# Kernel optimization log

Hardware: AMD Instinct MI355X
Metric: run time of the kernel (lower is better)

The kernel has to match this reference:

```python
import jax, jax.numpy as jnp
import numpy as np

N = 100000
E = 1600000
IN_C, HID_C, OUT_C = 512, 128, 40
K = 5
ALPHA = 0.5


def setup_inputs() -> dict:
    key = jax.random.key(0)
    k1, k2, k3, k4, k5, k6 = jax.random.split(key, 6)
    x = jax.random.normal(k1, (N, IN_C), dtype=jnp.float32)
    edge_index = jax.random.randint(k2, (2, E), 0, N, dtype=jnp.int64)
    # lin1: in -> hidden, lin2: hidden -> out (Kaiming-uniform-ish scale)
    W1 = jax.random.normal(k3, (IN_C, HID_C), dtype=jnp.float32) * (1.0 / np.sqrt(IN_C))
    b1 = jax.random.normal(k4, (HID_C,), dtype=jnp.float32) * 0.01
    W2 = jax.random.normal(k5, (HID_C, OUT_C), dtype=jnp.float32) * (1.0 / np.sqrt(HID_C))
    b2 = jax.random.normal(k6, (OUT_C,), dtype=jnp.float32) * 0.01
    return {"x": x, "edge_index": edge_index, "W1": W1, "b1": b1, "W2": W2, "b2": b2}


def _gcn_norm(edge_index, num_nodes):
    # add self-loops with weight 1, then symmetric normalization D^-1/2 A D^-1/2
    loops = jnp.arange(num_nodes, dtype=edge_index.dtype)
    row = jnp.concatenate([edge_index[0], loops])
    col = jnp.concatenate([edge_index[1], loops])
    w = jnp.ones(row.shape[0], dtype=jnp.float32)
    deg = jax.ops.segment_sum(w, col, num_segments=num_nodes)
    dinv = jnp.where(deg > 0, jax.lax.rsqrt(deg), 0.0)
    norm = dinv[row] * w * dinv[col]
    return row, col, norm


def reference(x, edge_index, W1, b1, W2, b2):
    h = x @ W1 + b1                      # [N, HID_C]
    row, col, norm = _gcn_norm(edge_index, N)
    x0 = h
    for _ in range(K):
        # gather source features, scale by edge norm, scatter-add to targets
        agg = jax.ops.segment_sum(norm[:, None] * h[row], col, num_segments=N)
        h = (1.0 - ALPHA) * agg + ALPHA * x0
    return h @ W2 + b2                   # [N, OUT_C]
```

## Files before the change

### kernel.cpp

```cpp
#include <hip/hip_runtime.h>
#include <hip/hip_bf16.h>

#define NN 100000
#define EE 1600000
#define HALFN 50000

typedef __attribute__((ext_vector_type(8))) short short8;
typedef __attribute__((ext_vector_type(4))) float f32x4;

__device__ __forceinline__ short f2bf(float f) {
    __hip_bfloat16 h = __float2bfloat16(f);
    return *reinterpret_cast<short*>(&h);
}
__device__ __forceinline__ float bf2f(unsigned short u) {
    return __uint_as_float((unsigned int)u << 16);
}


__global__ void wct_kernel(const float* __restrict__ W1, const float* __restrict__ W2,
                           const float* __restrict__ b1, short* __restrict__ WcT,
                           float* __restrict__ bc) {
    int t = blockIdx.x * 256 + threadIdx.x;
    if (t < 48 * 512) {
        int j = t >> 9, k = t & 511;
        float s = 0.f;
        if (j < 40)
            for (int i = 0; i < 128; ++i) s = fmaf(W1[k * 128 + i], W2[i * 40 + j], s);
        WcT[j * 512 + k] = f2bf(s);
    } else if (t < 48 * 512 + 48) {
        int j = t - 48 * 512;
        float s = 0.f;
        if (j < 40)
            for (int i = 0; i < 128; ++i) s = fmaf(b1[i], W2[i * 40 + j], s);
        bc[j] = s;
    }
}

__global__ __launch_bounds__(256) void gemm_z0(const float* __restrict__ x,
                                               const short* __restrict__ WcT,
                                               const float* __restrict__ bc,
                                               unsigned short* __restrict__ z0) {
    const int tid = threadIdx.x;
    const int lane = tid & 63;
    const int wave = tid >> 6;
    const int rbase = blockIdx.x * 64 + wave * 16;
    const int row = rbase + (lane & 15);
    const int kc = lane >> 4;
    const bool rok = row < NN;

    f32x4 acc0 = {0.f, 0.f, 0.f, 0.f};
    f32x4 acc1 = {0.f, 0.f, 0.f, 0.f};
    f32x4 acc2 = {0.f, 0.f, 0.f, 0.f};

    const float* xrow = x + (size_t)row * 512 + kc * 8;
    const short* bp0 = WcT + (size_t)(lane & 15) * 512 + kc * 8;
    const short* bp1 = bp0 + 16 * 512;
    const short* bp2 = bp0 + 32 * 512;

    for (int k0 = 0; k0 < 512; k0 += 32) {
        float4 p0 = {0.f, 0.f, 0.f, 0.f}, p1 = {0.f, 0.f, 0.f, 0.f};
        if (rok) {
            p0 = *reinterpret_cast<const float4*>(xrow + k0);
            p1 = *reinterpret_cast<const float4*>(xrow + k0 + 4);
        }
        short8 a;
        a[0] = f2bf(p0.x); a[1] = f2bf(p0.y); a[2] = f2bf(p0.z); a[3] = f2bf(p0.w);
        a[4] = f2bf(p1.x); a[5] = f2bf(p1.y); a[6] = f2bf(p1.z); a[7] = f2bf(p1.w);
        short8 b0 = *reinterpret_cast<const short8*>(bp0 + k0);
        short8 b1 = *reinterpret_cast<const short8*>(bp1 + k0);
        short8 b2 = *reinterpret_cast<const short8*>(bp2 + k0);
        acc0 = __builtin_amdgcn_mfma_f32_16x16x32_bf16(a, b0, acc0, 0, 0, 0);
        acc1 = __builtin_amdgcn_mfma_f32_16x16x32_bf16(a, b1, acc1, 0, 0, 0);
        acc2 = __builtin_amdgcn_mfma_f32_16x16x32_bf16(a, b2, acc2, 0, 0, 0);
    }

    const int cb = lane & 15;
    const int rr = rbase + (lane >> 4) * 4;
#pragma unroll
    for (int q = 0; q < 4; ++q) {
        int r = rr + q;
        if (r < NN) {
            z0[(size_t)r * 64 + cb] = (unsigned short)f2bf(acc0[q] + bc[cb]);
            z0[(size_t)r * 64 + cb + 16] = (unsigned short)f2bf(acc1[q] + bc[cb + 16]);
            z0[(size_t)r * 64 + cb + 32] = (unsigned short)f2bf(acc2[q] + bc[cb + 32]);
        }
    }
}

__global__ void count_kernel(const int* __restrict__ eidx, int* __restrict__ counts) {
    int e = blockIdx.x * 256 + threadIdx.x;
    if (e < EE) atomicAdd(&counts[eidx[EE + e]], 1);
}

__global__ void scan1(const int* __restrict__ counts, int* __restrict__ ptr,
                      int* __restrict__ bsum) {
    __shared__ int s[256];
    int tid = threadIdx.x;
    int i = blockIdx.x * 256 + tid;
    int v = (i < NN) ? counts[i] : 0;
    s[tid] = v;
    __syncthreads();
    for (int off = 1; off < 256; off <<= 1) {
        int t = (tid >= off) ? s[tid - off] : 0;
        __syncthreads();
        s[tid] += t;
        __syncthreads();
    }
    if (i < NN) ptr[i] = s[tid] - v;
    if (tid == 255) bsum[blockIdx.x] = s[255];
}

__global__ void scan2(int* __restrict__ bsum) {
    __shared__ int s[512];
    int tid = threadIdx.x;
    int v = (tid < 391) ? bsum[tid] : 0;
    s[tid] = v;
    __syncthreads();
    for (int off = 1; off < 512; off <<= 1) {
        int t = (tid >= off) ? s[tid - off] : 0;
        __syncthreads();
        s[tid] += t;
        __syncthreads();
    }
    if (tid < 391) bsum[tid] = s[tid] - v;
}

__global__ void scan3(int* __restrict__ ptr, const int* __restrict__ bsum,
                      const int* __restrict__ counts, float* __restrict__ dinvp) {
    int i = blockIdx.x * 256 + threadIdx.x;
    if (i < NN) {
        ptr[i] += bsum[blockIdx.x];
        dinvp[i] = rsqrtf(1.0f + (float)counts[i]);
    }
    if (i == 0) ptr[NN] = EE;
}

__global__ void scatter_kernel(const int* __restrict__ eidx, const int* __restrict__ ptr,
                               const float* __restrict__ dinvp, int* __restrict__ cursor,
                               int2* __restrict__ cev) {
    int e = blockIdx.x * 256 + threadIdx.x;
    if (e < EE) {
        int r = eidx[e];
        int c = eidx[EE + e];
        int pos = ptr[c] + atomicAdd(&cursor[c], 1);
        cev[pos] = make_int2(r, __float_as_int(dinvp[r]));
    }
}

__global__ __launch_bounds__(256) void propagate(const unsigned short* __restrict__ zcur,
                                                 const unsigned short* __restrict__ z0q,
                                                 unsigned short* __restrict__ znb,
                                                 float* __restrict__ outf,
                                                 const int* __restrict__ ptr,
                                                 const int2* __restrict__ cev,
                                                 const float* __restrict__ dinvp,
                                                 const float* __restrict__ b2, int last) {
    const int lane = threadIdx.x & 63;
    const int wid = blockIdx.x * 4 + (threadIdx.x >> 6);
    const int n0 = wid, n1 = wid + HALFN;

    const int beg0 = ptr[n0], end0 = ptr[n0 + 1];
    const int beg1 = ptr[n1], end1 = ptr[n1 + 1];
    const float dc0 = dinvp[n0], dc1 = dinvp[n1];

    int m0 = end0 - beg0; if (m0 > 64) m0 = 64;
    int m1 = end1 - beg1; if (m1 > 64) m1 = 64;
    int2 ev0 = make_int2(0, 0), ev1 = make_int2(0, 0);
    if (m0 > 0) ev0 = cev[beg0 + (lane < m0 ? lane : m0 - 1)];
    if (m1 > 0) ev1 = cev[beg1 + (lane < m1 ? lane : m1 - 1)];
    const float self0 = bf2f(zcur[(size_t)n0 * 64 + lane]);
    const float self1 = bf2f(zcur[(size_t)n1 * 64 + lane]);
    const float z00 = bf2f(z0q[(size_t)n0 * 64 + lane]);
    const float z01 = bf2f(z0q[(size_t)n1 * 64 + lane]);

    auto run_node = [&](int beg, int end, int2 ev, int m, float accInit) -> float {
        float a = accInit, b = 0.f;
        int e = beg;
        while (m > 0) {
            int rl = ev.x, vl = ev.y;
            int j = 0;
            for (; j + 4 <= m; j += 4) {
                int r0 = __builtin_amdgcn_readlane(rl, j + 0);
                int r1 = __builtin_amdgcn_readlane(rl, j + 1);
                int r2 = __builtin_amdgcn_readlane(rl, j + 2);
                int r3 = __builtin_amdgcn_readlane(rl, j + 3);
                float x0 = bf2f(zcur[(size_t)r0 * 64 + lane]);
                float x1 = bf2f(zcur[(size_t)r1 * 64 + lane]);
                float x2 = bf2f(zcur[(size_t)r2 * 64 + lane]);
                float x3 = bf2f(zcur[(size_t)r3 * 64 + lane]);
                float v0 = __int_as_float(__builtin_amdgcn_readlane(vl, j + 0));
                float v1 = __int_as_float(__builtin_amdgcn_readlane(vl, j + 1));
                float v2 = __int_as_float(__builtin_amdgcn_readlane(vl, j + 2));
                float v3 = __int_as_float(__builtin_amdgcn_readlane(vl, j + 3));
                a = fmaf(v0, x0, a);
                b = fmaf(v1, x1, b);
                a = fmaf(v2, x2, a);
                b = fmaf(v3, x3, b);
            }
            for (; j < m; ++j) {
                int r = __builtin_amdgcn_readlane(rl, j);
                float v = __int_as_float(__builtin_amdgcn_readlane(vl, j));
                a = fmaf(v, bf2f(zcur[(size_t)r * 64 + lane]), a);
            }
            e += m;
            m = end - e;
            if (m > 64) m = 64;
            if (m > 0) ev = cev[e + (lane < m ? lane : m - 1)];
        }
        return a + b;
    };

    float s0 = run_node(beg0, end0, ev0, m0, dc0 * self0);
    float res0 = 0.5f * dc0 * s0 + 0.5f * z00;
    if (last) {
        if (lane < 40) outf[(size_t)n0 * 40 + lane] = res0 + b2[lane];
    } else {
        znb[(size_t)n0 * 64 + lane] = (unsigned short)f2bf(res0);
    }

    float s1 = run_node(beg1, end1, ev1, m1, dc1 * self1);
    float res1 = 0.5f * dc1 * s1 + 0.5f * z01;
    if (last) {
        if (lane < 40) outf[(size_t)n1 * 40 + lane] = res1 + b2[lane];
    } else {
        znb[(size_t)n1 * 64 + lane] = (unsigned short)f2bf(res1);
    }
}

extern "C" void kernel_launch(void* const* d_in, const int* in_sizes, int n_in,
                              void* d_out, int out_size, void* d_ws, size_t ws_size,
                              hipStream_t stream) {
    const float* x  = (const float*)d_in[0];
    const int*   ei = (const int*)d_in[1];
    const float* W1 = (const float*)d_in[2];
    const float* b1 = (const float*)d_in[3];
    const float* W2 = (const float*)d_in[4];
    const float* b2 = (const float*)d_in[5];
    float* out = (float*)d_out;

    char* ws = (char*)d_ws;
    short*          WcT  = (short*)(ws + 0);
    float*          bc   = (float*)(ws + 49152);
    unsigned short* z0   = (unsigned short*)(ws + 65536);
    unsigned short* za   = (unsigned short*)(ws + 12865536);
    unsigned short* zb   = (unsigned short*)(ws + 25665536);
    float*          dinv = (float*)(ws + 38465536);
    int*            cnt  = (int*)(ws + 38865536);
    int*            ptr  = (int*)(ws + 39265536);
    int*            bsum = (int*)(ws + 39665664);
    int2*           cev  = (int2*)(ws + 39667712);

    hipMemsetAsync(cnt, 0, NN * sizeof(int), stream);
    wct_kernel<<<97, 256, 0, stream>>>(W1, W2, b1, WcT, bc);
    count_kernel<<<(EE + 255) / 256, 256, 0, stream>>>(ei, cnt);
    scan1<<<391, 256, 0, stream>>>(cnt, ptr, bsum);
    scan2<<<1, 512, 0, stream>>>(bsum);
    scan3<<<391, 256, 0, stream>>>(ptr, bsum, cnt, dinv);
    gemm_z0<<<1563, 256, 0, stream>>>(x, WcT, bc, z0);
    hipMemsetAsync(cnt, 0, NN * sizeof(int), stream);
    scatter_kernel<<<(EE + 255) / 256, 256, 0, stream>>>(ei, ptr, dinv, cnt, cev);

    propagate<<<12500, 256, 0, stream>>>(z0, z0, zb, out, ptr, cev, dinv, b2, 0);
    propagate<<<12500, 256, 0, stream>>>(zb, z0, za, out, ptr, cev, dinv, b2, 0);
    propagate<<<12500, 256, 0, stream>>>(za, z0, zb, out, ptr, cev, dinv, b2, 0);
    propagate<<<12500, 256, 0, stream>>>(zb, z0, za, out, ptr, cev, dinv, b2, 0);
    propagate<<<12500, 256, 0, stream>>>(za, z0, zb, out, ptr, cev, dinv, b2, 1);
}
```

Before: 469.3 us.

## Interleave two nodes' gathers in propagate and simplify CSR scatter cursors

The propagate kernel now processes both of its nodes together in chunks of 8 edges. It issues 16 independent row gathers before accumulating, so more loads are in flight per wave. Padding lanes get zero weight, so the loop runs to the longer node's chunk count. Degrees above 64 fall to a slow per-edge tail loop. Separately, the scatter step uses a copy of the row pointers as an atomic cursor, removing the second memset and the extra ptr read per edge.

```diff
diff --git a/kernel.cpp b/kernel.cpp
--- a/kernel.cpp
+++ b/kernel.cpp
@@ -126,23 +126,26 @@
 }
 
 __global__ void scan3(int* __restrict__ ptr, const int* __restrict__ bsum,
-                      const int* __restrict__ counts, float* __restrict__ dinvp) {
+                      const int* __restrict__ counts, float* __restrict__ dinvp,
+                      int* __restrict__ ptr2) {
     int i = blockIdx.x * 256 + threadIdx.x;
     if (i < NN) {
-        ptr[i] += bsum[blockIdx.x];
+        int p = ptr[i] + bsum[blockIdx.x];
+        ptr[i] = p;
+        ptr2[i] = p;
         dinvp[i] = rsqrtf(1.0f + (float)counts[i]);
     }
-    if (i == 0) ptr[NN] = EE;
-}
-
-__global__ void scatter_kernel(const int* __restrict__ eidx, const int* __restrict__ ptr,
-                               const float* __restrict__ dinvp, int* __restrict__ cursor,
+    if (i == 0) { ptr[NN] = EE; ptr2[NN] = EE; }
+}
+
+__global__ void scatter_kernel(const int* __restrict__ eidx,
+                               const float* __restrict__ dinvp, int* __restrict__ ptr2,
                                int2* __restrict__ cev) {
     int e = blockIdx.x * 256 + threadIdx.x;
     if (e < EE) {
         int r = eidx[e];
         int c = eidx[EE + e];
-        int pos = ptr[c] + atomicAdd(&cursor[c], 1);
+        int pos = atomicAdd(&ptr2[c], 1);
         cev[pos] = make_int2(r, __float_as_int(dinvp[r]));
     }
 }
@@ -159,70 +162,69 @@
     const int wid = blockIdx.x * 4 + (threadIdx.x >> 6);
     const int n0 = wid, n1 = wid + HALFN;
 
-    const int beg0 = ptr[n0], end0 = ptr[n0 + 1];
-    const int beg1 = ptr[n1], end1 = ptr[n1 + 1];
+    int beg0 = __builtin_amdgcn_readfirstlane(ptr[n0]);
+    int end0 = __builtin_amdgcn_readfirstlane(ptr[n0 + 1]);
+    int beg1 = __builtin_amdgcn_readfirstlane(ptr[n1]);
+    int end1 = __builtin_amdgcn_readfirstlane(ptr[n1 + 1]);
     const float dc0 = dinvp[n0], dc1 = dinvp[n1];
 
     int m0 = end0 - beg0; if (m0 > 64) m0 = 64;
     int m1 = end1 - beg1; if (m1 > 64) m1 = 64;
-    int2 ev0 = make_int2(0, 0), ev1 = make_int2(0, 0);
-    if (m0 > 0) ev0 = cev[beg0 + (lane < m0 ? lane : m0 - 1)];
-    if (m1 > 0) ev1 = cev[beg1 + (lane < m1 ? lane : m1 - 1)];
+
+    int idx0 = beg0 + (lane < m0 ? lane : m0 - 1); if (idx0 < 0) idx0 = 0;
+    int idx1 = beg1 + (lane < m1 ? lane : m1 - 1); if (idx1 < 0) idx1 = 0;
+    int2 ev0 = cev[idx0];
+    int2 ev1 = cev[idx1];
+    if (lane >= m0) ev0.y = 0;
+    if (lane >= m1) ev1.y = 0;
+
     const float self0 = bf2f(zcur[(size_t)n0 * 64 + lane]);
     const float self1 = bf2f(zcur[(size_t)n1 * 64 + lane]);
     const float z00 = bf2f(z0q[(size_t)n0 * 64 + lane]);
     const float z01 = bf2f(z0q[(size_t)n1 * 64 + lane]);
 
-    auto run_node = [&](int beg, int end, int2 ev, int m, float accInit) -> float {
-        float a = accInit, b = 0.f;
-        int e = beg;
-        while (m > 0) {
-            int rl = ev.x, vl = ev.y;
-            int j = 0;
-            for (; j + 4 <= m; j += 4) {
-                int r0 = __builtin_amdgcn_readlane(rl, j + 0);
-                int r1 = __builtin_amdgcn_readlane(rl, j + 1);
-                int r2 = __builtin_amdgcn_readlane(rl, j + 2);
-                int r3 = __builtin_amdgcn_readlane(rl, j + 3);
-                float x0 = bf2f(zcur[(size_t)r0 * 64 + lane]);
-                float x1 = bf2f(zcur[(size_t)r1 * 64 + lane]);
-                float x2 = bf2f(zcur[(size_t)r2 * 64 + lane]);
-                float x3 = bf2f(zcur[(size_t)r3 * 64 + lane]);
-                float v0 = __int_as_float(__builtin_amdgcn_readlane(vl, j + 0));
-                float v1 = __int_as_float(__builtin_amdgcn_readlane(vl, j + 1));
-                float v2 = __int_as_float(__builtin_amdgcn_readlane(vl, j + 2));
-                float v3 = __int_as_float(__builtin_amdgcn_readlane(vl, j + 3));
-                a = fmaf(v0, x0, a);
-                b = fmaf(v1, x1, b);
-                a = fmaf(v2, x2, a);
-                b = fmaf(v3, x3, b);
-            }
-            for (; j < m; ++j) {
-                int r = __builtin_amdgcn_readlane(rl, j);
-                float v = __int_as_float(__builtin_amdgcn_readlane(vl, j));
-                a = fmaf(v, bf2f(zcur[(size_t)r * 64 + lane]), a);
-            }
-            e += m;
-            m = end - e;
-            if (m > 64) m = 64;
-            if (m > 0) ev = cev[e + (lane < m ? lane : m - 1)];
-        }
-        return a + b;
-    };
-
-    float s0 = run_node(beg0, end0, ev0, m0, dc0 * self0);
-    float res0 = 0.5f * dc0 * s0 + 0.5f * z00;
+    float A0 = dc0 * self0, B0 = 0.f;
+    float A1 = dc1 * self1, B1 = 0.f;
+
+    int nc0 = (m0 + 7) >> 3, nc1 = (m1 + 7) >> 3;
+    int nc = nc0 > nc1 ? nc0 : nc1;
+    for (int c = 0; c < nc; ++c) {
+        const int j = c * 8;
+        float x[8], y[8];
+#pragma unroll
+        for (int k = 0; k < 8; ++k) {
+            int r0 = __builtin_amdgcn_readlane(ev0.x, j + k);
+            int r1 = __builtin_amdgcn_readlane(ev1.x, j + k);
+            x[k] = bf2f(zcur[(size_t)r0 * 64 + lane]);
+            y[k] = bf2f(zcur[(size_t)r1 * 64 + lane]);
+        }
+#pragma unroll
+        for (int k = 0; k < 8; ++k) {
+            float w = __int_as_float(__builtin_amdgcn_readlane(ev0.y, j + k));
+            float u = __int_as_float(__builtin_amdgcn_readlane(ev1.y, j + k));
+            if (k & 1) { B0 = fmaf(w, x[k], B0); B1 = fmaf(u, y[k], B1); }
+            else       { A0 = fmaf(w, x[k], A0); A1 = fmaf(u, y[k], A1); }
+        }
+    }
+
+    for (int e = beg0 + 64; e < end0; ++e) {
+        int2 ee = cev[e];
+        A0 = fmaf(__int_as_float(ee.y), bf2f(zcur[(size_t)ee.x * 64 + lane]), A0);
+    }
+    for (int e = beg1 + 64; e < end1; ++e) {
+        int2 ee = cev[e];
+        A1 = fmaf(__int_as_float(ee.y), bf2f(zcur[(size_t)ee.x * 64 + lane]), A1);
+    }
+
+    float res0 = 0.5f * dc0 * (A0 + B0) + 0.5f * z00;
+    float res1 = 0.5f * dc1 * (A1 + B1) + 0.5f * z01;
     if (last) {
-        if (lane < 40) outf[(size_t)n0 * 40 + lane] = res0 + b2[lane];
+        if (lane < 40) {
+            outf[(size_t)n0 * 40 + lane] = res0 + b2[lane];
+            outf[(size_t)n1 * 40 + lane] = res1 + b2[lane];
+        }
     } else {
         znb[(size_t)n0 * 64 + lane] = (unsigned short)f2bf(res0);
-    }
-
-    float s1 = run_node(beg1, end1, ev1, m1, dc1 * self1);
-    float res1 = 0.5f * dc1 * s1 + 0.5f * z01;
-    if (last) {
-        if (lane < 40) outf[(size_t)n1 * 40 + lane] = res1 + b2[lane];
-    } else {
         znb[(size_t)n1 * 64 + lane] = (unsigned short)f2bf(res1);
     }
 }
@@ -248,17 +250,17 @@
     int*            cnt  = (int*)(ws + 38865536);
     int*            ptr  = (int*)(ws + 39265536);
     int*            bsum = (int*)(ws + 39665664);
-    int2*           cev  = (int2*)(ws + 39667712);
+    int*            ptr2 = (int*)(ws + 39667712);
+    int2*           cev  = (int2*)(ws + 40067840);
 
     hipMemsetAsync(cnt, 0, NN * sizeof(int), stream);
     wct_kernel<<<97, 256, 0, stream>>>(W1, W2, b1, WcT, bc);
     count_kernel<<<(EE + 255) / 256, 256, 0, stream>>>(ei, cnt);
     scan1<<<391, 256, 0, stream>>>(cnt, ptr, bsum);
     scan2<<<1, 512, 0, stream>>>(bsum);
-    scan3<<<391, 256, 0, stream>>>(ptr, bsum, cnt, dinv);
+    scan3<<<391, 256, 0, stream>>>(ptr, bsum, cnt, dinv, ptr2);
     gemm_z0<<<1563, 256, 0, stream>>>(x, WcT, bc, z0);
-    hipMemsetAsync(cnt, 0, NN * sizeof(int), stream);
-    scatter_kernel<<<(EE + 255) / 256, 256, 0, stream>>>(ei, ptr, dinv, cnt, cev);
+    scatter_kernel<<<(EE + 255) / 256, 256, 0, stream>>>(ei, dinv, ptr2, cev);
 
     propagate<<<12500, 256, 0, stream>>>(z0, z0, zb, out, ptr, cev, dinv, b2, 0);
     propagate<<<12500, 256, 0, stream>>>(zb, z0, za, out, ptr, cev, dinv, b2, 0);
```

New measurement: 426.8 us. 9.1% less time.
